# Kernel optimization log

Hardware: AMD Instinct MI355X
Metric: run time of the kernel (lower is better)

The kernel has to match this reference:

```python
import jax, jax.numpy as jnp
import numpy as np

HEADS = 12
DIM = 768


def setup_inputs() -> dict:
    key = jax.random.key(0)
    ks = jax.random.split(key, 4)
    s = 0.02
    return {
        "x": jax.random.normal(ks[0], (8, 64, 64, DIM), dtype=jnp.float32),
        "w_qkv_h": jax.random.normal(ks[1], (DIM, 3 * DIM), dtype=jnp.float32) * s,
        "b_qkv_h": jnp.zeros((3 * DIM,), jnp.float32),
        "w_qkv_w": jax.random.normal(ks[2], (DIM, 3 * DIM), dtype=jnp.float32) * s,
        "b_qkv_w": jnp.zeros((3 * DIM,), jnp.float32),
        "w_proj": jax.random.normal(ks[3], (DIM, DIM), dtype=jnp.float32) * s,
        "b_proj": jnp.zeros((DIM,), jnp.float32),
    }


def _axial_attn(x_seq, w, b, heads, scale):
    # x_seq: [N, L, C]. Faithful to original torch code: q,k,v keep shape
    # [N, L, heads, hd]; matmul contracts hd, producing [N, L, heads, heads]
    # attention ACROSS HEADS at each position (no head permute in the source).
    N, L, C = x_seq.shape
    hd = C // heads
    qkv = (x_seq @ w + b).reshape(N, L, 3, heads, hd)
    q = qkv[:, :, 0] * scale
    k = qkv[:, :, 1]
    v = qkv[:, :, 2]
    attn = jax.nn.softmax(jnp.einsum('nlhd,nlgd->nlhg', q, k), axis=-1)
    out = jnp.einsum('nlhg,nlgd->nlhd', attn, v)
    return out.reshape(N, L, C)


def reference(x, w_qkv_h, b_qkv_h, w_qkv_w, b_qkv_w, w_proj, b_proj):
    B, H, W, C = x.shape
    scale = (C // HEADS) ** -0.5
    # H-axis pass: permute to [B, W, H, C], flatten batch*W
    x_h = jnp.transpose(x, (0, 2, 1, 3)).reshape(B * W, H, C)
    out_h = _axial_attn(x_h, w_qkv_h, b_qkv_h, HEADS, scale)
    out_h = jnp.transpose(out_h.reshape(B, W, H, C), (0, 2, 1, 3))
    # W-axis pass: flatten batch*H
    out_w = _axial_attn(x.reshape(B * H, W, C), w_qkv_w, b_qkv_w, HEADS, scale)
    out_w = out_w.reshape(B, H, W, C)
    # residual-style sum of the two axes, then output projection (dropout p=0)
    return (out_h + out_w) @ w_proj + b_proj
```

## Files before the change

### kernel.cpp

```cpp
#include <hip/hip_runtime.h>

typedef unsigned short u16;
typedef unsigned int u32;
typedef __attribute__((ext_vector_type(8))) short short8;
typedef __attribute__((ext_vector_type(4))) float f32x4;

#define DIMC 768
#define NQKV 2304
#define NPOS 32768
#define NKT 12

__device__ __forceinline__ float b2f(u16 u) {
    union { u32 i; float f; } c; c.i = ((u32)u) << 16; return c.f;
}
__device__ __forceinline__ u16 f2b(float f) {
    union { float f; u32 i; } c; c.f = f;
    u32 r = c.i + 0x7fffu + ((c.i >> 16) & 1u);
    return (u16)(r >> 16);
}

__device__ __forceinline__ void gl_lds16(const void* g, void* l) {
    __builtin_amdgcn_global_load_lds(
        (const __attribute__((address_space(1))) void*)g,
        (__attribute__((address_space(3))) void*)l, 16, 0, 0);
}

__global__ __launch_bounds__(256) void cvt_bf16(
    const float* __restrict__ in, u16* __restrict__ out, int n4)
{
    int i = blockIdx.x * 256 + threadIdx.x;
    if (i >= n4) return;
    float4 v = ((const float4*)in)[i];
    ushort4 o;
    o.x = f2b(v.x); o.y = f2b(v.y); o.z = f2b(v.z); o.w = f2b(v.w);
    ((ushort4*)out)[i] = o;
}

__global__ __launch_bounds__(256) void cvt_wT(
    const float* __restrict__ W0, const float* __restrict__ W1,
    const float* __restrict__ W2,
    u16* __restrict__ T0, u16* __restrict__ T1, u16* __restrict__ T2)
{
    const int z = blockIdx.z;
    const float* W = (z == 0) ? W0 : (z == 1) ? W1 : W2;
    u16* WT = (z == 0) ? T0 : (z == 1) ? T1 : T2;
    const int N = (z == 2) ? 768 : 2304;
    const int nb = blockIdx.x, kb = blockIdx.y;
    if (nb * 64 >= N) return;
    __shared__ u16 T[64][65];
    const int t = threadIdx.x, sr = t >> 2, sc = t & 3;
    {
        const float4* p = (const float4*)(W + (size_t)(kb * 64 + sr) * N + nb * 64 + sc * 16);
        float4 a0 = p[0], a1 = p[1], a2 = p[2], a3 = p[3];
        float vv[16] = {a0.x, a0.y, a0.z, a0.w, a1.x, a1.y, a1.z, a1.w,
                        a2.x, a2.y, a2.z, a2.w, a3.x, a3.y, a3.z, a3.w};
        #pragma unroll
        for (int i = 0; i < 16; ++i)
            T[sc * 16 + i][sr] = f2b(vv[i]);
    }
    __syncthreads();
    {
        u16 vv[16];
        #pragma unroll
        for (int i = 0; i < 16; ++i) vv[i] = T[sr][sc * 16 + i];
        uint4 p0, p1;
        p0.x = vv[0] | ((u32)vv[1] << 16);  p0.y = vv[2] | ((u32)vv[3] << 16);
        p0.z = vv[4] | ((u32)vv[5] << 16);  p0.w = vv[6] | ((u32)vv[7] << 16);
        p1.x = vv[8] | ((u32)vv[9] << 16);  p1.y = vv[10] | ((u32)vv[11] << 16);
        p1.z = vv[12] | ((u32)vv[13] << 16); p1.w = vv[14] | ((u32)vv[15] << 16);
        u16* q = WT + (size_t)(nb * 64 + sr) * DIMC + kb * 64 + sc * 16;
        *(uint4*)q = p0;
        *(uint4*)(q + 8) = p1;
    }
}


#define STAGE_A(buf, kt, ht) do {                                              \
    gl_lds16(aS + (size_t)((ht) * 128)      * DIMC + (size_t)(kt) * 64,        \
             &As[buf][(ht) * 8192 +        w * 512]);                          \
    gl_lds16(aS + (size_t)((ht) * 128 + 64) * DIMC + (size_t)(kt) * 64,        \
             &As[buf][(ht) * 8192 + 4096 + w * 512]);                          \
} while (0)

#define STAGE_B(buf, kt, ht) do {                                              \
    gl_lds16(bS + (size_t)((ht) * 128)      * DIMC + (size_t)(kt) * 64,        \
             &Bs[buf][(ht) * 8192 +        w * 512]);                          \
    gl_lds16(bS + (size_t)((ht) * 128 + 64) * DIMC + (size_t)(kt) * 64,        \
             &Bs[buf][(ht) * 8192 + 4096 + w * 512]);                          \
} while (0)

#define READ_A(base, hm) do {                                                  \
    _Pragma("unroll")                                                          \
    for (int i_ = 0; i_ < 4; ++i_) {                                           \
        const int row_ = (hm) * 128 + wm * 64 + i_ * 16 + lr;                  \
        _Pragma("unroll")                                                      \
        for (int ks_ = 0; ks_ < 2; ++ks_)                                      \
            af[i_][ks_] = *(const short8*)((base) + (row_ << 6) +              \
                              (((ks_ * 4 + lq) ^ (row_ & 7)) << 3));           \
    }                                                                          \
} while (0)

#define READ_B(dst, base, hn) do {                                             \
    _Pragma("unroll")                                                          \
    for (int j_ = 0; j_ < 2; ++j_) {                                           \
        const int row_ = (hn) * 128 + wn * 32 + j_ * 16 + lr;                  \
        _Pragma("unroll")                                                      \
        for (int ks_ = 0; ks_ < 2; ++ks_)                                      \
            (dst)[j_][ks_] = *(const short8*)((base) + (row_ << 6) +           \
                              (((ks_ * 4 + lq) ^ (row_ & 7)) << 3));           \
    }                                                                          \
} while (0)

#define MM(hm, hn, bsrc) do {                                                  \
    __builtin_amdgcn_s_setprio(1);                                             \
    _Pragma("unroll")                                                          \
    for (int i_ = 0; i_ < 4; ++i_)                                             \
        _Pragma("unroll")                                                      \
        for (int j_ = 0; j_ < 2; ++j_)                                         \
            _Pragma("unroll")                                                  \
            for (int ks_ = 0; ks_ < 2; ++ks_)                                  \
                acc[(hm) * 4 + i_][(hn) * 2 + j_] =                            \
                    __builtin_amdgcn_mfma_f32_16x16x32_bf16(                   \
                        af[i_][ks_], (bsrc)[j_][ks_],                          \
                        acc[(hm) * 4 + i_][(hn) * 2 + j_], 0, 0, 0);           \
    __builtin_amdgcn_s_setprio(0);                                             \
} while (0)

#define PBAR() do {                                                            \
    __builtin_amdgcn_sched_barrier(0);                                         \
    __builtin_amdgcn_s_barrier();                                              \
    __builtin_amdgcn_sched_barrier(0);                                         \
} while (0)

#define KTILE(kt, STG) do {                                                    \
    const int p_ = (kt) & 1, q_ = p_ ^ 1;                                      \
    const u16* Ab_ = As[p_];                                                   \
    const u16* Bb_ = Bs[p_];                                                   \
                                                            \
    if (STG) { STAGE_A(q_, (kt) + 1, 0); STAGE_B(q_, (kt) + 1, 0); }           \
    READ_A(Ab_, 0);                                                            \
    READ_B(b1, Bb_, 1);                                                        \
    PBAR();                                                                    \
    MM(0, 0, b0);                                                              \
                                                            \
    if (STG) { STAGE_B(q_, (kt) + 1, 1); STAGE_A(q_, (kt) + 1, 1); }           \
    PBAR();                                                                    \
    MM(0, 1, b1);                                                              \
    READ_A(Ab_, 1);                \
                                                            \
    asm volatile("s_waitcnt vmcnt(4)" ::: "memory");                           \
    PBAR();                                                                    \
    MM(1, 0, b0);                                                              \
                                                            \
    if (STG) READ_B(b0, Bs[q_], 0);   \
    asm volatile("s_waitcnt vmcnt(0)" ::: "memory");                           \
    PBAR();                                                                    \
    MM(1, 1, b1);                                                              \
} while (0)

__global__ __launch_bounds__(512, 2) void gemm256(
    const u16* __restrict__ A, const u16* __restrict__ BT,
    const float* __restrict__ bias, void* __restrict__ C,
    int ldn, int c_is_f32)
{
    __shared__ __align__(16) u16 As[2][256 * 64];
    __shared__ __align__(16) u16 Bs[2][256 * 64];

    const int t = threadIdx.x;
    const int w = t >> 6, l = t & 63;
    const int wm = w >> 2, wn = w & 3;
    const int lr = l & 15, lq = l >> 4;

    const int gx = (int)gridDim.x;
    const int nwg = gx * (int)gridDim.y;
    const int lin = (int)blockIdx.y * gx + (int)blockIdx.x;
    const int swz = (lin & 7) * (nwg >> 3) + (lin >> 3);
    const int by = swz / gx, bx = swz - by * gx;
    const int mBase = by * 256, nBase = bx * 256;

    const int srow = t >> 3;
    const int schk = (t & 7) ^ (srow & 7);
    const u16* aS = A  + (size_t)(mBase + srow) * DIMC + schk * 8;
    const u16* bS = BT + (size_t)(nBase + srow) * DIMC + schk * 8;

    f32x4 acc[8][4];
    #pragma unroll
    for (int i = 0; i < 8; ++i)
        #pragma unroll
        for (int j = 0; j < 4; ++j)
            acc[i][j] = (f32x4){0.f, 0.f, 0.f, 0.f};

    short8 af[4][2], b0[2][2], b1[2][2];

    STAGE_A(0, 0, 0); STAGE_B(0, 0, 0); STAGE_B(0, 0, 1); STAGE_A(0, 0, 1);
    asm volatile("s_waitcnt vmcnt(0)" ::: "memory");
    PBAR();
    READ_B(b0, Bs[0], 0);

    #pragma unroll 1
    for (int kt = 0; kt < NKT - 1; ++kt) { KTILE(kt, 1); }
    { KTILE(NKT - 1, 0); }

    #pragma unroll
    for (int hn = 0; hn < 2; ++hn)
        #pragma unroll
        for (int j = 0; j < 2; ++j) {
            const int col = nBase + hn * 128 + wn * 32 + j * 16 + lr;
            const float bb = bias[col];
            #pragma unroll
            for (int hm = 0; hm < 2; ++hm)
                #pragma unroll
                for (int i = 0; i < 4; ++i) {
                    const int row = mBase + hm * 128 + wm * 64 + i * 16 + lq * 4;
                    #pragma unroll
                    for (int rg = 0; rg < 4; ++rg) {
                        float v = acc[hm * 4 + i][hn * 2 + j][rg] + bb;
                        size_t idx = (size_t)(row + rg) * ldn + col;
                        if (c_is_f32) ((float*)C)[idx] = v;
                        else          ((u16*)C)[idx]   = f2b(v);
                    }
                }
        }
}

__global__ __launch_bounds__(256) void headattn(
    const u16* __restrict__ qkv, u16* __restrict__ sum, int accumulate)
{
    __shared__ float qs[4][12 * 65];
    __shared__ float ks[4][12 * 65];
    __shared__ float vs[4][12 * 65];
    __shared__ float Sld[4][144];
    const int t = threadIdx.x, wv = t >> 6, lane = t & 63;
    const int p = blockIdx.x * 4 + wv;
    const u16* row = qkv + (size_t)p * NQKV;

    #pragma unroll
    for (int j = 0; j < 9; ++j) {
        int u2 = lane + 64 * j;
        uint2 d2 = *(const uint2*)(row + u2 * 4);
        int c = u2 * 4;
        int s = c / 768, rr = c % 768;
        int h = rr >> 6, d = rr & 63;
        float* dst = (s == 0) ? qs[wv] : (s == 1) ? ks[wv] : vs[wv];
        dst[h * 65 + d + 0] = b2f((u16)(d2.x & 0xffffu));
        dst[h * 65 + d + 1] = b2f((u16)(d2.x >> 16));
        dst[h * 65 + d + 2] = b2f((u16)(d2.y & 0xffffu));
        dst[h * 65 + d + 3] = b2f((u16)(d2.y >> 16));
    }
    __syncthreads();
    for (int e = lane; e < 144; e += 64) {
        int h = e / 12, g = e - h * 12;
        float s = 0.f;
        #pragma unroll 8
        for (int d = 0; d < 64; ++d)
            s = fmaf(qs[wv][h * 65 + d], ks[wv][g * 65 + d], s);
        Sld[wv][e] = s * 0.125f;
    }
    __syncthreads();
    if (lane < 12) {
        float m = -1e30f;
        #pragma unroll
        for (int g = 0; g < 12; ++g) m = fmaxf(m, Sld[wv][lane * 12 + g]);
        float ex[12]; float ssum = 0.f;
        #pragma unroll
        for (int g = 0; g < 12; ++g) { ex[g] = __expf(Sld[wv][lane * 12 + g] - m); ssum += ex[g]; }
        float inv = 1.f / ssum;
        #pragma unroll
        for (int g = 0; g < 12; ++g) Sld[wv][lane * 12 + g] = ex[g] * inv;
    }
    __syncthreads();
    u16* orow = sum + (size_t)p * DIMC;
    #pragma unroll
    for (int h = 0; h < 12; ++h) {
        float o = 0.f;
        #pragma unroll
        for (int g = 0; g < 12; ++g)
            o = fmaf(Sld[wv][h * 12 + g], vs[wv][g * 65 + lane], o);
        int idx = h * 64 + lane;
        if (accumulate) o += b2f(orow[idx]);
        orow[idx] = f2b(o);
    }
}

extern "C" void kernel_launch(void* const* d_in, const int* in_sizes, int n_in,
                              void* d_out, int out_size, void* d_ws, size_t ws_size,
                              hipStream_t stream) {
    const float* x  = (const float*)d_in[0];
    const float* wh = (const float*)d_in[1];
    const float* bh = (const float*)d_in[2];
    const float* ww = (const float*)d_in[3];
    const float* bw = (const float*)d_in[4];
    const float* wp = (const float*)d_in[5];
    const float* bp = (const float*)d_in[6];
    float* out = (float*)d_out;

    u16* xb   = (u16*)d_ws;
    u16* whT  = xb   + 25165824;
    u16* wwT  = whT  + 1769472;
    u16* wpT  = wwT  + 1769472;
    u16* qkvb = wpT  + 589824;
    u16* sumb = qkvb + 75497472;

    cvt_bf16<<<24576, 256, 0, stream>>>(x, xb, 6291456);
    dim3 wg(36, 12, 3);
    cvt_wT<<<wg, 256, 0, stream>>>(wh, ww, wp, whT, wwT, wpT);

    dim3 gq(NQKV / 256, NPOS / 256);
    dim3 gp(DIMC / 256, NPOS / 256);

    gemm256<<<gq, 512, 0, stream>>>(xb, whT, bh, qkvb, NQKV, 0);
    headattn<<<NPOS / 4, 256, 0, stream>>>(qkvb, sumb, 0);
    gemm256<<<gq, 512, 0, stream>>>(xb, wwT, bw, qkvb, NQKV, 0);
    headattn<<<NPOS / 4, 256, 0, stream>>>(qkvb, sumb, 1);
    gemm256<<<gp, 512, 0, stream>>>(sumb, wpT, bp, out, DIMC, 1);
}
```

Baseline: 727.6 us.

## Deepen GEMM prefetch pipeline and move head attention onto MFMA

The GEMM k-loop is rescheduled so that stages for the tile two ahead are issued into the current buffer halves, with a relaxed vmcnt wait. The goal is to hide more global-load latency behind the MFMAs. Separately, the per-position cross-head attention kernel is rewritten to compute QK^T and PV with bf16 MFMA instructions and a shuffle-based softmax, replacing scalar fp32 LDS loops and block-wide syncs. The attention rewrite adds bf16 rounding of the probabilities and relies on zero-padding the 12×12 problem up to 16×16 tiles.

```diff
diff --git a/kernel.cpp b/kernel.cpp
--- a/kernel.cpp
+++ b/kernel.cpp
@@ -126,35 +126,37 @@
     __builtin_amdgcn_s_setprio(0);                                             \
 } while (0)
 
-#define PBAR() do {                                                            \
+#define BAR() do {                                                             \
     __builtin_amdgcn_sched_barrier(0);                                         \
     __builtin_amdgcn_s_barrier();                                              \
     __builtin_amdgcn_sched_barrier(0);                                         \
 } while (0)
 
-#define KTILE(kt, STG) do {                                                    \
+#define KTILE(kt, S12, S34, VN) do {                                           \
     const int p_ = (kt) & 1, q_ = p_ ^ 1;                                      \
     const u16* Ab_ = As[p_];                                                   \
     const u16* Bb_ = Bs[p_];                                                   \
-                                                            \
-    if (STG) { STAGE_A(q_, (kt) + 1, 0); STAGE_B(q_, (kt) + 1, 0); }           \
+                                                             \
     READ_A(Ab_, 0);                                                            \
+    READ_B(b0, Bb_, 0);                                                        \
+    if (S12) STAGE_B(q_, (kt) + 1, 1);                                         \
+    BAR();                                                                     \
+    MM(0, 0, b0);                                                              \
+                                                             \
     READ_B(b1, Bb_, 1);                                                        \
-    PBAR();                                                                    \
-    MM(0, 0, b0);                                                              \
-                                                            \
-    if (STG) { STAGE_B(q_, (kt) + 1, 1); STAGE_A(q_, (kt) + 1, 1); }           \
-    PBAR();                                                                    \
+    if (S12) STAGE_A(q_, (kt) + 1, 1);                                         \
+    BAR();                                                                     \
     MM(0, 1, b1);                                                              \
-    READ_A(Ab_, 1);                \
-                                                            \
-    asm volatile("s_waitcnt vmcnt(4)" ::: "memory");                           \
-    PBAR();                                                                    \
+                                                             \
+    READ_A(Ab_, 1);                                                            \
+    if (S34) STAGE_A(p_, (kt) + 2, 0);                                         \
+    BAR();                                                                     \
     MM(1, 0, b0);                                                              \
-                                                            \
-    if (STG) READ_B(b0, Bs[q_], 0);   \
-    asm volatile("s_waitcnt vmcnt(0)" ::: "memory");                           \
-    PBAR();                                                                    \
+                                                             \
+    if (S34) STAGE_B(p_, (kt) + 2, 0);                                         \
+    __builtin_amdgcn_sched_barrier(0);                                         \
+    asm volatile("s_waitcnt vmcnt(" VN ")" ::: "memory");                      \
+    BAR();                                                                     \
     MM(1, 1, b1);                                                              \
 } while (0)
 
@@ -193,13 +195,15 @@
     short8 af[4][2], b0[2][2], b1[2][2];
 
     STAGE_A(0, 0, 0); STAGE_B(0, 0, 0); STAGE_B(0, 0, 1); STAGE_A(0, 0, 1);
-    asm volatile("s_waitcnt vmcnt(0)" ::: "memory");
-    PBAR();
-    READ_B(b0, Bs[0], 0);
+    STAGE_A(1, 1, 0); STAGE_B(1, 1, 0);
+    __builtin_amdgcn_sched_barrier(0);
+    asm volatile("s_waitcnt vmcnt(4)" ::: "memory");
+    BAR();
 
     #pragma unroll 1
-    for (int kt = 0; kt < NKT - 1; ++kt) { KTILE(kt, 1); }
-    { KTILE(NKT - 1, 0); }
+    for (int kt = 0; kt < NKT - 2; ++kt) { KTILE(kt, 1, 1, "4"); }
+    { KTILE(NKT - 2, 1, 0, "0"); }
+    { KTILE(NKT - 1, 0, 0, "0"); }
 
     #pragma unroll
     for (int hn = 0; hn < 2; ++hn)
@@ -226,59 +230,78 @@
 __global__ __launch_bounds__(256) void headattn(
     const u16* __restrict__ qkv, u16* __restrict__ sum, int accumulate)
 {
-    __shared__ float qs[4][12 * 65];
-    __shared__ float ks[4][12 * 65];
-    __shared__ float vs[4][12 * 65];
-    __shared__ float Sld[4][144];
-    const int t = threadIdx.x, wv = t >> 6, lane = t & 63;
+    __shared__ u16 VtL[4][64 * 16];
+    __shared__ u16 PL[4][16 * 16];
+    const int t = threadIdx.x, wv = t >> 6, l = t & 63;
     const int p = blockIdx.x * 4 + wv;
     const u16* row = qkv + (size_t)p * NQKV;
+    const int lr = l & 15, lq = l >> 4;
+    u16* Vt = VtL[wv];
+    u16* P  = PL[wv];
+
+    short8 qa0 = *(const short8*)(row +       lr * 64 + lq * 8);
+    short8 qa1 = *(const short8*)(row +       lr * 64 + lq * 8 + 32);
+    short8 kb0 = *(const short8*)(row + 768 + lr * 64 + lq * 8);
+    short8 kb1 = *(const short8*)(row + 768 + lr * 64 + lq * 8 + 32);
+
+    *(uint2*)(Vt + l * 16 + 12) = (uint2){0u, 0u};
+    {
+        const int g = l >> 3, d0 = (l & 7) * 8;
+        short8 v = *(const short8*)(row + 1536 + g * 64 + d0);
+        #pragma unroll
+        for (int i = 0; i < 8; ++i) Vt[(d0 + i) * 16 + g] = (u16)v[i];
+        if (l < 32) {
+            const int g2 = 8 + (l >> 3);
+            short8 v2 = *(const short8*)(row + 1536 + g2 * 64 + d0);
+            #pragma unroll
+            for (int i = 0; i < 8; ++i) Vt[(d0 + i) * 16 + g2] = (u16)v2[i];
+        }
+    }
+
+    f32x4 s = (f32x4){0.f, 0.f, 0.f, 0.f};
+    s = __builtin_amdgcn_mfma_f32_16x16x32_bf16(qa0, kb0, s, 0, 0, 0);
+    s = __builtin_amdgcn_mfma_f32_16x16x32_bf16(qa1, kb1, s, 0, 0, 0);
 
     #pragma unroll
-    for (int j = 0; j < 9; ++j) {
-        int u2 = lane + 64 * j;
-        uint2 d2 = *(const uint2*)(row + u2 * 4);
-        int c = u2 * 4;
-        int s = c / 768, rr = c % 768;
-        int h = rr >> 6, d = rr & 63;
-        float* dst = (s == 0) ? qs[wv] : (s == 1) ? ks[wv] : vs[wv];
-        dst[h * 65 + d + 0] = b2f((u16)(d2.x & 0xffffu));
-        dst[h * 65 + d + 1] = b2f((u16)(d2.x >> 16));
-        dst[h * 65 + d + 2] = b2f((u16)(d2.y & 0xffffu));
-        dst[h * 65 + d + 3] = b2f((u16)(d2.y >> 16));
-    }
-    __syncthreads();
-    for (int e = lane; e < 144; e += 64) {
-        int h = e / 12, g = e - h * 12;
-        float s = 0.f;
-        #pragma unroll 8
-        for (int d = 0; d < 64; ++d)
-            s = fmaf(qs[wv][h * 65 + d], ks[wv][g * 65 + d], s);
-        Sld[wv][e] = s * 0.125f;
-    }
-    __syncthreads();
-    if (lane < 12) {
-        float m = -1e30f;
-        #pragma unroll
-        for (int g = 0; g < 12; ++g) m = fmaxf(m, Sld[wv][lane * 12 + g]);
-        float ex[12]; float ssum = 0.f;
-        #pragma unroll
-        for (int g = 0; g < 12; ++g) { ex[g] = __expf(Sld[wv][lane * 12 + g] - m); ssum += ex[g]; }
-        float inv = 1.f / ssum;
-        #pragma unroll
-        for (int g = 0; g < 12; ++g) Sld[wv][lane * 12 + g] = ex[g] * inv;
-    }
-    __syncthreads();
-    u16* orow = sum + (size_t)p * DIMC;
+    for (int rg = 0; rg < 4; ++rg) {
+        float x = (lr < 12) ? s[rg] * 0.125f : -1e30f;
+        float m = x;
+        m = fmaxf(m, __shfl_xor(m, 1));
+        m = fmaxf(m, __shfl_xor(m, 2));
+        m = fmaxf(m, __shfl_xor(m, 4));
+        m = fmaxf(m, __shfl_xor(m, 8));
+        float e = (lr < 12) ? __expf(x - m) : 0.f;
+        float ss = e;
+        ss += __shfl_xor(ss, 1);
+        ss += __shfl_xor(ss, 2);
+        ss += __shfl_xor(ss, 4);
+        ss += __shfl_xor(ss, 8);
+        P[(lq * 4 + rg) * 16 + lr] = f2b(e / ss);
+    }
+
+    const short8 z8 = (short8){0, 0, 0, 0, 0, 0, 0, 0};
+    short8 pa = z8;
+    if (lq < 2) pa = *(const short8*)(P + lr * 16 + lq * 8);
+    f32x4 o[4];
     #pragma unroll
-    for (int h = 0; h < 12; ++h) {
-        float o = 0.f;
-        #pragma unroll
-        for (int g = 0; g < 12; ++g)
-            o = fmaf(Sld[wv][h * 12 + g], vs[wv][g * 65 + lane], o);
-        int idx = h * 64 + lane;
-        if (accumulate) o += b2f(orow[idx]);
-        orow[idx] = f2b(o);
+    for (int c = 0; c < 4; ++c) {
+        short8 vb = z8;
+        if (lq < 2) vb = *(const short8*)(Vt + (c * 16 + lr) * 16 + lq * 8);
+        f32x4 a0 = (f32x4){0.f, 0.f, 0.f, 0.f};
+        o[c] = __builtin_amdgcn_mfma_f32_16x16x32_bf16(pa, vb, a0, 0, 0, 0);
+    }
+
+    if (lq < 3) {
+        u16* orow = sum + (size_t)p * DIMC;
+        #pragma unroll
+        for (int c = 0; c < 4; ++c)
+            #pragma unroll
+            for (int rg = 0; rg < 4; ++rg) {
+                const int idx = (lq * 4 + rg) * 64 + c * 16 + lr;
+                float v = o[c][rg];
+                if (accumulate) v += b2f(orow[idx]);
+                orow[idx] = f2b(v);
+            }
     }
 }
 
```

New measurement: 585.1 us. -19.6%, faster.
